# Performance work log

Measured on AMD Instinct MI355X. Metric: run time of the kernel, lower is better.

The kernel has to match this reference:

```python
import jax, jax.numpy as jnp
import numpy as np

NUM_LAYERS = 4
NUM_HEADS = 8
D_MODEL = 256
D_FF = 1024
UNC_THRESHOLD = 0.3
B, L = 2, 2048


def _layer_norm(x, g, b, eps=1e-5):
    m = jnp.mean(x, axis=-1, keepdims=True)
    v = jnp.mean((x - m) ** 2, axis=-1, keepdims=True)
    return (x - m) * jax.lax.rsqrt(v + eps) * g + b


def setup_inputs() -> dict:
    key = jax.random.key(0)
    ks = jax.random.split(key, 32)
    D, F, Ly = D_MODEL, D_FF, NUM_LAYERS
    w = lambda k, shape: jax.random.normal(k, shape, dtype=jnp.float32) * 0.02
    return {
        'x': jax.random.normal(ks[0], (B, L, D), dtype=jnp.float32),
        'Win': w(ks[1], (D, D)), 'bin_': jnp.zeros((D,), jnp.float32),
        'Wq': w(ks[2], (Ly, D, D)), 'bq': jnp.zeros((Ly, D), jnp.float32),
        'Wk': w(ks[3], (Ly, D, D)), 'bk': jnp.zeros((Ly, D), jnp.float32),
        'Wv': w(ks[4], (Ly, D, D)), 'bv': jnp.zeros((Ly, D), jnp.float32),
        'Wo': w(ks[5], (Ly, D, D)), 'bo': jnp.zeros((Ly, D), jnp.float32),
        'ev_scale': jnp.ones((Ly,), jnp.float32),
        'ev_bias': jnp.zeros((Ly,), jnp.float32),
        'W1': w(ks[6], (Ly, D, F)), 'b1': jnp.zeros((Ly, F), jnp.float32),
        'W2': w(ks[7], (Ly, F, D)), 'b2': jnp.zeros((Ly, D), jnp.float32),
        'n1g': jnp.ones((Ly, D), jnp.float32), 'n1b': jnp.zeros((Ly, D), jnp.float32),
        'n2g': jnp.ones((Ly, D), jnp.float32), 'n2b': jnp.zeros((Ly, D), jnp.float32),
        'fng': jnp.ones((D,), jnp.float32), 'fnb': jnp.zeros((D,), jnp.float32),
        'Wout': w(ks[8], (D, D)), 'bout': jnp.zeros((D,), jnp.float32),
    }


def _evidence_attention(x, Wq, bq, Wk, bk, Wv, bv, Wo, bo, scale, bias):
    b, l, d = x.shape
    hd = d // NUM_HEADS
    def heads(t):
        return t.reshape(b, l, NUM_HEADS, hd).transpose(0, 2, 1, 3)  # [B,H,L,hd]
    Q = heads(x @ Wq + bq)
    K = heads(x @ Wk + bk)
    V = heads(x @ Wv + bv)
    scores = jnp.einsum('bhqd,bhkd->bhqk', Q, K) / np.sqrt(hd).astype(np.float32)
    evidence = jnp.exp(scores) * scale + 1.0 + bias           # [B,H,L,L]
    denom = jnp.sum(evidence, axis=-1, keepdims=True)         # [B,H,L,1]
    uncertainty = (jnp.float32(l) / denom)[..., 0]            # [B,H,L]
    probs = evidence / denom
    attn = jnp.einsum('bhqk,bhkd->bhqd', probs, V)
    attn = attn.transpose(0, 2, 1, 3).reshape(b, l, d)
    return attn @ Wo + bo, uncertainty


def reference(x, Win, bin_, Wq, bq, Wk, bk, Wv, bv, Wo, bo, ev_scale, ev_bias,
              W1, b1, W2, b2, n1g, n1b, n2g, n2b, fng, fnb, Wout, bout):
    h = x @ Win + bin_
    total_unc = 0.0
    for i in range(NUM_LAYERS):
        attn_out, unc = _evidence_attention(
            _layer_norm(h, n1g[i], n1b[i]),
            Wq[i], bq[i], Wk[i], bk[i], Wv[i], bv[i], Wo[i], bo[i],
            ev_scale[i], ev_bias[i])
        h = h + attn_out
        ff = jax.nn.gelu(_layer_norm(h, n2g[i], n2b[i]) @ W1[i] + b1[i], approximate=False) @ W2[i] + b2[i]
        h = h + ff
        total_unc = total_unc + unc
    avg_unc = total_unc / NUM_LAYERS                          # [B,H,L]
    out = _layer_norm(h, fng, fnb) @ Wout + bout              # [B,L,D]
    should_abstain = avg_unc > UNC_THRESHOLD
    return out, avg_unc, should_abstain
```

## Files before the change

### kernel.cpp

```cpp
#include <hip/hip_runtime.h>
#include <hip/hip_bf16.h>
#include <math.h>

#define B_  2
#define L_  2048
#define D_  256
#define H_  8
#define HD_ 32
#define F_  1024
#define LY_ 4
#define M_  (B_*L_)

typedef __attribute__((ext_vector_type(8))) short bf16x8;
typedef __attribute__((ext_vector_type(4))) float f32x4;

static __device__ __forceinline__ short f2bf(float f) {
    return __builtin_bit_cast(short, __float2bfloat16(f));
}

static __device__ __forceinline__ void gload_lds16(const ushort* g, ushort* l) {
    __builtin_amdgcn_global_load_lds(
        (const __attribute__((address_space(1))) void*)g,
        (__attribute__((address_space(3))) void*)l, 16, 0, 0);
}

__global__ __launch_bounds__(256) void transpose_weights(
    const float* __restrict__ Win, const float* __restrict__ Wq,
    const float* __restrict__ Wk,  const float* __restrict__ Wv,
    const float* __restrict__ Wo,  const float* __restrict__ W1,
    const float* __restrict__ W2,  const float* __restrict__ Wout,
    ushort* __restrict__ T)
{
    const int bid = blockIdx.x;
    const float* src; ushort* dst; int K, N, tt;
    if (bid < 64)        { src = Win; dst = T; K = 256; N = 256; tt = bid; }
    else if (bid < 1088) {
        int i = bid - 64; int which = i >> 8; int l = (i >> 6) & 3; tt = i & 63;
        K = 256; N = 256;
        const float* s4[4] = {Wq, Wk, Wv, Wo};
        src = s4[which] + l * 65536;
        dst = T + 65536 * (1 + which * 4 + l);
    } else if (bid < 2112) {
        int i = bid - 1088; int l = i >> 8; tt = i & 255; K = 256; N = 1024;
        src = W1 + l * 262144; dst = T + 65536 * 17 + l * 262144;
    } else if (bid < 3136) {
        int i = bid - 2112; int l = i >> 8; tt = i & 255; K = 1024; N = 256;
        src = W2 + l * 262144; dst = T + 65536 * 17 + 1048576 + l * 262144;
    } else {
        src = Wout; dst = T + 65536 * 17 + 2097152; K = 256; N = 256; tt = bid - 3136;
    }
    const int ntn = N >> 5;
    const int tk = tt / ntn, tn = tt % ntn;
    __shared__ float ld[32][33];
    const int t = threadIdx.x;
    const int r = t >> 3, c4 = (t & 7) * 4;
    float4 v = *reinterpret_cast<const float4*>(&src[(size_t)(tk * 32 + r) * N + tn * 32 + c4]);
    ld[r][c4 + 0] = v.x; ld[r][c4 + 1] = v.y; ld[r][c4 + 2] = v.z; ld[r][c4 + 3] = v.w;
    __syncthreads();
    short4 o;
    o.x = f2bf(ld[c4 + 0][r]);
    o.y = f2bf(ld[c4 + 1][r]);
    o.z = f2bf(ld[c4 + 2][r]);
    o.w = f2bf(ld[c4 + 3][r]);
    *reinterpret_cast<short4*>(&dst[(size_t)(tn * 32 + r) * K + tk * 32 + c4]) = o;
}

__device__ __forceinline__ void gemm_core64(
    const ushort* __restrict__ A, const ushort* __restrict__ Wt, int K,
    int row0, int col0, ushort* sA, ushort* sW, f32x4 acc[2][2])
{
    const int tid  = threadIdx.x;
    const int lane = tid & 63;
    const int wid  = tid >> 6;
    const int wr = wid >> 1, wc = wid & 1;
    const int g = lane >> 4, nn = lane & 15;

    const int r0 = tid >> 3;
    const int sx = ((tid & 7) ^ (r0 & 7)) << 3;

    const ushort* Ap = &A[(size_t)(row0 + r0) * K + sx];
    const ushort* Wp = &Wt[(size_t)(col0 + r0) * K + sx];
    const size_t rstep = (size_t)32 * K;

    ushort* ldsA = sA + wid * 512;
    ushort* ldsW = sW + wid * 512;

    gload_lds16(Ap,         ldsA);
    gload_lds16(Ap + rstep, ldsA + 2048);
    gload_lds16(Wp,         ldsW);
    gload_lds16(Wp + rstep, ldsW + 2048);

    const int ra = (wr * 32 + nn) * 64, rb = ra + 16 * 64;
    const int rc = (wc * 32 + nn) * 64, rd = rc + 16 * 64;
    const int m7 = nn & 7;

    int cur = 0;
    __syncthreads();
    for (int k0 = 0; k0 < K; k0 += 64) {
        if (k0 + 64 < K) {
            ushort* lA = ldsA + (cur ^ 1) * 4096;
            ushort* lW = ldsW + (cur ^ 1) * 4096;
            gload_lds16(Ap + k0 + 64,         lA);
            gload_lds16(Ap + k0 + 64 + rstep, lA + 2048);
            gload_lds16(Wp + k0 + 64,         lW);
            gload_lds16(Wp + k0 + 64 + rstep, lW + 2048);
        }
        const ushort* a = sA + cur * 4096;
        const ushort* w = sW + cur * 4096;
#pragma unroll
        for (int sk = 0; sk < 2; ++sk) {
            const int sw = ((sk * 4 + g) ^ m7) << 3;
            bf16x8 a0 = *reinterpret_cast<const bf16x8*>(&a[ra + sw]);
            bf16x8 a1 = *reinterpret_cast<const bf16x8*>(&a[rb + sw]);
            bf16x8 w0 = *reinterpret_cast<const bf16x8*>(&w[rc + sw]);
            bf16x8 w1 = *reinterpret_cast<const bf16x8*>(&w[rd + sw]);
            acc[0][0] = __builtin_amdgcn_mfma_f32_16x16x32_bf16(a0, w0, acc[0][0], 0, 0, 0);
            acc[0][1] = __builtin_amdgcn_mfma_f32_16x16x32_bf16(a0, w1, acc[0][1], 0, 0, 0);
            acc[1][0] = __builtin_amdgcn_mfma_f32_16x16x32_bf16(a1, w0, acc[1][0], 0, 0, 0);
            acc[1][1] = __builtin_amdgcn_mfma_f32_16x16x32_bf16(a1, w1, acc[1][1], 0, 0, 0);
        }
        __syncthreads();
        cur ^= 1;
    }
}

__global__ __launch_bounds__(256) void gemm_first(
    const float* __restrict__ Hin, const ushort* __restrict__ Wt,
    const float* __restrict__ bias, float* __restrict__ Cout)
{
    __shared__ __align__(16) ushort sLN[64 * 264];
    __shared__ __align__(16) ushort sW[2 * 4096];
    const int row0 = blockIdx.y * 64, col0 = blockIdx.x * 64;
    const int tid  = threadIdx.x;
    const int lane = tid & 63;
    const int wid  = tid >> 6;
    const int wr = wid >> 1, wc = wid & 1;
    const int g = lane >> 4, nn = lane & 15;

    const int r0 = tid >> 3;
    const int sx = ((tid & 7) ^ (r0 & 7)) << 3;
    const ushort* Wp = &Wt[(size_t)(col0 + r0) * 256 + sx];
    ushort* ldsW = sW + wid * 512;
    gload_lds16(Wp,            ldsW);
    gload_lds16(Wp + 32 * 256, ldsW + 2048);

    const float4* hp = reinterpret_cast<const float4*>(Hin + (size_t)row0 * D_);
#pragma unroll
    for (int j = 0; j < 16; ++j) {
        const float4 v = hp[j * 256 + tid];
        short4 o = {f2bf(v.x), f2bf(v.y), f2bf(v.z), f2bf(v.w)};
        *reinterpret_cast<short4*>(&sLN[(j * 4 + wid) * 264 + lane * 4]) = o;
    }
    __syncthreads();

    const int ra = (wr * 32 + nn) * 264, rb = ra + 16 * 264;
    const int rc = (wc * 32 + nn) * 64,  rd = rc + 16 * 64;
    const int m7 = nn & 7;
    f32x4 acc[2][2] = {};

    int cur = 0;
#pragma unroll
    for (int k0 = 0; k0 < 256; k0 += 64) {
        if (k0 + 64 < 256) {
            ushort* lW = ldsW + (cur ^ 1) * 4096;
            gload_lds16(Wp + k0 + 64,            lW);
            gload_lds16(Wp + k0 + 64 + 32 * 256, lW + 2048);
        }
        const ushort* w = sW + cur * 4096;
#pragma unroll
        for (int sk = 0; sk < 2; ++sk) {
            const int ac = k0 + sk * 32 + g * 8;
            bf16x8 a0 = *reinterpret_cast<const bf16x8*>(&sLN[ra + ac]);
            bf16x8 a1 = *reinterpret_cast<const bf16x8*>(&sLN[rb + ac]);
            const int sw = ((sk * 4 + g) ^ m7) << 3;
            bf16x8 w0 = *reinterpret_cast<const bf16x8*>(&w[rc + sw]);
            bf16x8 w1 = *reinterpret_cast<const bf16x8*>(&w[rd + sw]);
            acc[0][0] = __builtin_amdgcn_mfma_f32_16x16x32_bf16(a0, w0, acc[0][0], 0, 0, 0);
            acc[0][1] = __builtin_amdgcn_mfma_f32_16x16x32_bf16(a0, w1, acc[0][1], 0, 0, 0);
            acc[1][0] = __builtin_amdgcn_mfma_f32_16x16x32_bf16(a1, w0, acc[1][0], 0, 0, 0);
            acc[1][1] = __builtin_amdgcn_mfma_f32_16x16x32_bf16(a1, w1, acc[1][1], 0, 0, 0);
        }
        __syncthreads();
        cur ^= 1;
    }

#pragma unroll
    for (int mi = 0; mi < 2; ++mi)
#pragma unroll
    for (int ni = 0; ni < 2; ++ni)
#pragma unroll
    for (int r = 0; r < 4; ++r) {
        const int m = row0 + wr * 32 + mi * 16 + g * 4 + r;
        const int c = col0 + wc * 32 + ni * 16 + nn;
        Cout[(size_t)m * D_ + c] = acc[mi][ni][r] + bias[c];
    }
}

__device__ __forceinline__ void gemm_core32(
    const ushort* __restrict__ A, const ushort* __restrict__ Wt, int K,
    int row0, int col0, ushort* sA, ushort* sW, f32x4 acc[2])
{
    const int tid  = threadIdx.x;
    const int lane = tid & 63;
    const int wid  = tid >> 6;
    const int wr = wid >> 1, wc = wid & 1;
    const int g = lane >> 4, nn = lane & 15;

    const int r0 = tid >> 3;
    const int sx = ((tid & 7) ^ (r0 & 7)) << 3;

    const ushort* Ap = &A[(size_t)(row0 + r0) * K + sx];
    const ushort* Wp = &Wt[(size_t)(col0 + r0) * K + sx];
    const size_t rstep = (size_t)32 * K;

    ushort* ldsA = sA + wid * 512;
    ushort* ldsW = sW + wid * 512;

    gload_lds16(Ap,         ldsA);
    gload_lds16(Wp,         ldsW);
    gload_lds16(Wp + rstep, ldsW + 2048);

    const int ra = (wr * 16 + nn) * 64;
    const int rc = (wc * 32 + nn) * 64, rd = rc + 16 * 64;
    const int m7 = nn & 7;

    int cur = 0;
    __syncthreads();
    for (int k0 = 0; k0 < K; k0 += 64) {
        if (k0 + 64 < K) {
            ushort* lA = ldsA + (cur ^ 1) * 2048;
            ushort* lW = ldsW + (cur ^ 1) * 4096;
            gload_lds16(Ap + k0 + 64,         lA);
            gload_lds16(Wp + k0 + 64,         lW);
            gload_lds16(Wp + k0 + 64 + rstep, lW + 2048);
        }
        const ushort* a = sA + cur * 2048;
        const ushort* w = sW + cur * 4096;
#pragma unroll
        for (int sk = 0; sk < 2; ++sk) {
            const int sw = ((sk * 4 + g) ^ m7) << 3;
            bf16x8 a0 = *reinterpret_cast<const bf16x8*>(&a[ra + sw]);
            bf16x8 w0 = *reinterpret_cast<const bf16x8*>(&w[rc + sw]);
            bf16x8 w1 = *reinterpret_cast<const bf16x8*>(&w[rd + sw]);
            acc[0] = __builtin_amdgcn_mfma_f32_16x16x32_bf16(a0, w0, acc[0], 0, 0, 0);
            acc[1] = __builtin_amdgcn_mfma_f32_16x16x32_bf16(a0, w1, acc[1], 0, 0, 0);
        }
        __syncthreads();
        cur ^= 1;
    }
}

__global__ __launch_bounds__(256) void gemm_res32(
    const ushort* __restrict__ A, const ushort* __restrict__ Wt,
    const float* __restrict__ bias, float* __restrict__ C, int K)
{
    __shared__ __align__(16) ushort sA[2 * 2048];
    __shared__ __align__(16) ushort sW[2 * 4096];
    const int row0 = blockIdx.y * 32, col0 = blockIdx.x * 64;
    f32x4 acc[2] = {};
    gemm_core32(A, Wt, K, row0, col0, sA, sW, acc);

    const int lane = threadIdx.x & 63;
    const int wid  = threadIdx.x >> 6;
    const int wr = wid >> 1, wc = wid & 1;
    const int g = lane >> 4, nn = lane & 15;
#pragma unroll
    for (int ni = 0; ni < 2; ++ni)
#pragma unroll
    for (int r = 0; r < 4; ++r) {
        const int m = row0 + wr * 16 + g * 4 + r;
        const int c = col0 + wc * 32 + ni * 16 + nn;
        C[(size_t)m * D_ + c] += acc[ni][r] + bias[c];
    }
}

__global__ __launch_bounds__(256) void gemm_out32(
    const ushort* __restrict__ A, const ushort* __restrict__ Wt,
    const float* __restrict__ bias, float* __restrict__ Cout)
{
    __shared__ __align__(16) ushort sA[2 * 2048];
    __shared__ __align__(16) ushort sW[2 * 4096];
    const int row0 = blockIdx.y * 32, col0 = blockIdx.x * 64;
    f32x4 acc[2] = {};
    gemm_core32(A, Wt, 256, row0, col0, sA, sW, acc);

    const int lane = threadIdx.x & 63;
    const int wid  = threadIdx.x >> 6;
    const int wr = wid >> 1, wc = wid & 1;
    const int g = lane >> 4, nn = lane & 15;
#pragma unroll
    for (int ni = 0; ni < 2; ++ni)
#pragma unroll
    for (int r = 0; r < 4; ++r) {
        const int m = row0 + wr * 16 + g * 4 + r;
        const int c = col0 + wc * 32 + ni * 16 + nn;
        Cout[(size_t)m * D_ + c] = acc[ni][r] + bias[c];
    }
}

template<int EPI, int OUTBF>
__global__ __launch_bounds__(256) void gemm_bf16(
    const ushort* __restrict__ A, const ushort* __restrict__ Wt,
    const float* __restrict__ bias, const float* __restrict__ res,
    void* __restrict__ Cout, int M, int N, int K)
{
    __shared__ __align__(16) ushort sA[2 * 4096];
    __shared__ __align__(16) ushort sW[2 * 4096];
    const int row0 = blockIdx.y * 64, col0 = blockIdx.x * 64;
    f32x4 acc[2][2] = {};
    gemm_core64(A, Wt, K, row0, col0, sA, sW, acc);

    const int lane = threadIdx.x & 63;
    const int wid  = threadIdx.x >> 6;
    const int wr = wid >> 1, wc = wid & 1;
    const int g = lane >> 4, nn = lane & 15;
#pragma unroll
    for (int mi = 0; mi < 2; ++mi)
#pragma unroll
    for (int ni = 0; ni < 2; ++ni)
#pragma unroll
    for (int r = 0; r < 4; ++r) {
        const int m = row0 + wr * 32 + mi * 16 + g * 4 + r;
        const int c = col0 + wc * 32 + ni * 16 + nn;
        float v = acc[mi][ni][r] + bias[c];
        if (EPI == 1) v = 0.5f * v * (1.0f + erff(v * 0.70710678118654752f));
        if (EPI == 2) v += res[(size_t)m * N + c];
        if (OUTBF) ((ushort*)Cout)[(size_t)m * N + c] = (ushort)f2bf(v);
        else       ((float*)Cout)[(size_t)m * N + c] = v;
    }
}

__global__ __launch_bounds__(256) void gemm_qkv(
    const ushort* __restrict__ A,
    const ushort* __restrict__ WqT, const ushort* __restrict__ WkT,
    const ushort* __restrict__ WvT,
    const float* __restrict__ bq, const float* __restrict__ bk,
    const float* __restrict__ bv,
    ushort* __restrict__ Qb, ushort* __restrict__ Kb, ushort* __restrict__ Vt)
{
    __shared__ __align__(16) ushort sA[2 * 4096];
    __shared__ __align__(16) ushort sW[2 * 4096];
    const int nb = blockIdx.x;
    const int wsel = nb >> 2;
    const int col0 = (nb & 3) * 64;
    const int row0 = blockIdx.y * 64;
    const ushort* Wt = (wsel == 0) ? WqT : (wsel == 1) ? WkT : WvT;
    const float* bias = (wsel == 0) ? bq : (wsel == 1) ? bk : bv;

    f32x4 acc[2][2] = {};
    gemm_core64(A, Wt, 256, row0, col0, sA, sW, acc);

    const int lane = threadIdx.x & 63;
    const int wid  = threadIdx.x >> 6;
    const int wr = wid >> 1, wc = wid & 1;
    const int g = lane >> 4, nn = lane & 15;
    ushort* QK = (wsel == 0) ? Qb : Kb;
#pragma unroll
    for (int mi = 0; mi < 2; ++mi)
#pragma unroll
    for (int ni = 0; ni < 2; ++ni)
#pragma unroll
    for (int r = 0; r < 4; ++r) {
        const int m = row0 + wr * 32 + mi * 16 + g * 4 + r;
        const int c = col0 + wc * 32 + ni * 16 + nn;
        const float v = acc[mi][ni][r] + bias[c];
        if (wsel < 2) {
            QK[(size_t)m * D_ + c] = (ushort)f2bf(v);
        } else {
            const int b = m >> 11, l = m & 2047;
            const int h = c >> 5,  d = c & 31;
            Vt[(size_t)((b * 8 + h) * 32 + d) * L_ + l] = (ushort)f2bf(v);
        }
    }
}

__global__ __launch_bounds__(256) void ln_kernel8(
    const float* __restrict__ x, const float* __restrict__ g,
    const float* __restrict__ b, ushort* __restrict__ y)
{
    const int tid  = threadIdx.x;
    const int row  = blockIdx.x * 8 + (tid >> 5);
    const int l    = tid & 31;
    const float* xp = x + (size_t)row * D_ + l * 8;

    float4 v0 = *reinterpret_cast<const float4*>(xp);
    float4 v1 = *reinterpret_cast<const float4*>(xp + 4);

    float s  = v0.x + v0.y + v0.z + v0.w + v1.x + v1.y + v1.z + v1.w;
    float s2 = v0.x*v0.x + v0.y*v0.y + v0.z*v0.z + v0.w*v0.w
             + v1.x*v1.x + v1.y*v1.y + v1.z*v1.z + v1.w*v1.w;
    s  += __shfl_xor(s, 1);  s  += __shfl_xor(s, 2);  s  += __shfl_xor(s, 4);
    s  += __shfl_xor(s, 8);  s  += __shfl_xor(s, 16);
    s2 += __shfl_xor(s2, 1); s2 += __shfl_xor(s2, 2); s2 += __shfl_xor(s2, 4);
    s2 += __shfl_xor(s2, 8); s2 += __shfl_xor(s2, 16);

    const float m   = s * (1.0f / D_);
    const float var = s2 * (1.0f / D_) - m * m;
    const float r   = rsqrtf(var + 1e-5f);

    const float4 g0 = reinterpret_cast<const float4*>(g)[l * 2];
    const float4 g1 = reinterpret_cast<const float4*>(g)[l * 2 + 1];
    const float4 b0 = reinterpret_cast<const float4*>(b)[l * 2];
    const float4 b1 = reinterpret_cast<const float4*>(b)[l * 2 + 1];

    short4 o0, o1;
    o0.x = f2bf((v0.x - m) * r * g0.x + b0.x);
    o0.y = f2bf((v0.y - m) * r * g0.y + b0.y);
    o0.z = f2bf((v0.z - m) * r * g0.z + b0.z);
    o0.w = f2bf((v0.w - m) * r * g0.w + b0.w);
    o1.x = f2bf((v1.x - m) * r * g1.x + b1.x);
    o1.y = f2bf((v1.y - m) * r * g1.y + b1.y);
    o1.z = f2bf((v1.z - m) * r * g1.z + b1.z);
    o1.w = f2bf((v1.w - m) * r * g1.w + b1.w);
    ushort* yp = y + (size_t)row * D_ + l * 8;
    *reinterpret_cast<short4*>(yp)     = o0;
    *reinterpret_cast<short4*>(yp + 4) = o1;
}

__global__ __launch_bounds__(256) void attn_mfma(
    const ushort* __restrict__ Qb, const ushort* __restrict__ Kb,
    const ushort* __restrict__ Vt, ushort* __restrict__ O,
    float* __restrict__ unc, const float* __restrict__ ev_scale,
    const float* __restrict__ ev_bias, int layer,
    float* __restrict__ out_unc, float* __restrict__ out_abst)
{
    const int bh = blockIdx.y;
    const int b  = bh >> 3;
    const int h  = bh & 7;
    const int tid  = threadIdx.x;
    const int wv   = tid >> 6;
    const int lane = tid & 63;
    const int g = lane >> 4;
    const int n = lane & 15;
    const int q  = blockIdx.x * 64 + wv * 16 + n;
    const float scale = ev_scale[layer];
    const float cb    = 1.0f + ev_bias[layer];
    const float isq   = 0.17677669529663687f;

    __shared__ __align__(16) ushort sK[2][64][40];
    __shared__ __align__(16) ushort sV[2][32][72];

    const size_t qk0 = (size_t)b * L_ * D_ + h * HD_;

    bf16x8 qf;
    {
        const bf16x8 qr = *reinterpret_cast<const bf16x8*>(&Qb[qk0 + (size_t)q * D_ + g * 8]);
#pragma unroll
        for (int j = 0; j < 8; ++j) {
            const float qv = __builtin_bit_cast(float, ((unsigned)(unsigned short)qr[j]) << 16);
            qf[j] = f2bf(qv * isq);
        }
    }
    bf16x8 ones;
#pragma unroll
    for (int j = 0; j < 8; ++j) ones[j] = (short)0x3F80;

    const int krow = tid >> 2, kch = (tid & 3) * 8;
    const int vrow = tid >> 3, vch = (tid & 7) * 8;
    const ushort* ksrc = Kb + qk0 + (size_t)krow * D_ + kch;
    const ushort* vsrc = Vt + (size_t)((b * 8 + h) * 32 + vrow) * L_ + vch;

    f32x4 acc0 = {0.f, 0.f, 0.f, 0.f};
    f32x4 acc1 = {0.f, 0.f, 0.f, 0.f};
    f32x4 accS = {0.f, 0.f, 0.f, 0.f};
    const f32x4 zero = {0.f, 0.f, 0.f, 0.f};

    bf16x8 kA = *reinterpret_cast<const bf16x8*>(ksrc);
    bf16x8 vA = *reinterpret_cast<const bf16x8*>(vsrc);
    bf16x8 kB = *reinterpret_cast<const bf16x8*>(ksrc + (size_t)64 * D_);
    bf16x8 vB = *reinterpret_cast<const bf16x8*>(vsrc + 64);

#define SYNC_BAR()                                                    \
    do {                                                              \
        asm volatile("s_waitcnt lgkmcnt(0)" ::: "memory");            \
        __builtin_amdgcn_s_barrier();                                 \
        asm volatile("" ::: "memory");                                \
    } while (0)

#define ATTN_TILE(BUF)                                                          \
    do {                                                                        \
        _Pragma("unroll")                                                       \
        for (int tt = 0; tt < 64; tt += 32) {                                   \
            bf16x8 kf0 = *reinterpret_cast<const bf16x8*>(&sK[BUF][tt + n][g * 8]);      \
            bf16x8 kf1 = *reinterpret_cast<const bf16x8*>(&sK[BUF][tt + 16 + n][g * 8]); \
            f32x4 s0 = __builtin_amdgcn_mfma_f32_16x16x32_bf16(kf0, qf, zero, 0, 0, 0);  \
            f32x4 s1 = __builtin_amdgcn_mfma_f32_16x16x32_bf16(kf1, qf, zero, 0, 0, 0);  \
            short4 va = *reinterpret_cast<const short4*>(&sV[BUF][n][tt + g * 4]);       \
            short4 vb = *reinterpret_cast<const short4*>(&sV[BUF][n][tt + 16 + g * 4]);  \
            short4 vc = *reinterpret_cast<const short4*>(&sV[BUF][n + 16][tt + g * 4]);  \
            short4 vd = *reinterpret_cast<const short4*>(&sV[BUF][n + 16][tt + 16 + g * 4]); \
            bf16x8 vf0 = {va.x, va.y, va.z, va.w, vb.x, vb.y, vb.z, vb.w};      \
            bf16x8 vf1 = {vc.x, vc.y, vc.z, vc.w, vd.x, vd.y, vd.z, vd.w};      \
            bf16x8 pa;                                                          \
            _Pragma("unroll")                                                   \
            for (int r = 0; r < 4; ++r) pa[r]     = f2bf(fmaf(__expf(s0[r]), scale, cb)); \
            _Pragma("unroll")                                                   \
            for (int r = 0; r < 4; ++r) pa[r + 4] = f2bf(fmaf(__expf(s1[r]), scale, cb)); \
            acc0 = __builtin_amdgcn_mfma_f32_16x16x32_bf16(vf0, pa, acc0, 0, 0, 0); \
            acc1 = __builtin_amdgcn_mfma_f32_16x16x32_bf16(vf1, pa, acc1, 0, 0, 0); \
            accS = __builtin_amdgcn_mfma_f32_16x16x32_bf16(ones, pa, accS, 0, 0, 0); \
        }                                                                       \
    } while (0)

    for (int t = 0; t < L_; t += 128) {
        *reinterpret_cast<bf16x8*>(&sK[0][krow][kch]) = kA;
        *reinterpret_cast<bf16x8*>(&sV[0][vrow][vch]) = vA;
        if (t + 128 < L_) {
            kA = *reinterpret_cast<const bf16x8*>(ksrc + (size_t)(t + 128) * D_);
            vA = *reinterpret_cast<const bf16x8*>(vsrc + (t + 128));
        }
        SYNC_BAR();
        ATTN_TILE(0);

        *reinterpret_cast<bf16x8*>(&sK[1][krow][kch]) = kB;
        *reinterpret_cast<bf16x8*>(&sV[1][vrow][vch]) = vB;
        if (t + 192 < L_) {
            kB = *reinterpret_cast<const bf16x8*>(ksrc + (size_t)(t + 192) * D_);
            vB = *reinterpret_cast<const bf16x8*>(vsrc + (t + 192));
        }
        SYNC_BAR();
        ATTN_TILE(1);
    }
#undef ATTN_TILE
#undef SYNC_BAR

    const float inv = 1.0f / accS[0];

    ushort* op = &O[qk0 + (size_t)q * D_ + g * 4];
    short4 o0 = {f2bf(acc0[0] * inv), f2bf(acc0[1] * inv), f2bf(acc0[2] * inv), f2bf(acc0[3] * inv)};
    short4 o1 = {f2bf(acc1[0] * inv), f2bf(acc1[1] * inv), f2bf(acc1[2] * inv), f2bf(acc1[3] * inv)};
    *reinterpret_cast<short4*>(op)      = o0;
    *reinterpret_cast<short4*>(op + 16) = o1;

    if (g == 0) {
        const float u = (float)L_ * inv;
        const int uidx = bh * L_ + q;
        if (layer == 0) {
            unc[uidx] = u;
        } else if (layer < LY_ - 1) {
            unc[uidx] += u;
        } else {
            const float avg = (unc[uidx] + u) * 0.25f;
            out_unc[uidx]  = avg;
            out_abst[uidx] = (avg > 0.3f) ? 1.0f : 0.0f;
        }
    }
}

extern "C" void kernel_launch(void* const* d_in, const int* in_sizes, int n_in,
                              void* d_out, int out_size, void* d_ws, size_t ws_size,
                              hipStream_t stream)
{
    const float* x    = (const float*)d_in[0];
    const float* Win  = (const float*)d_in[1];
    const float* bin_ = (const float*)d_in[2];
    const float* Wq   = (const float*)d_in[3];
    const float* bq   = (const float*)d_in[4];
    const float* Wk   = (const float*)d_in[5];
    const float* bk   = (const float*)d_in[6];
    const float* Wv   = (const float*)d_in[7];
    const float* bv   = (const float*)d_in[8];
    const float* Wo   = (const float*)d_in[9];
    const float* bo   = (const float*)d_in[10];
    const float* evs  = (const float*)d_in[11];
    const float* evb  = (const float*)d_in[12];
    const float* W1   = (const float*)d_in[13];
    const float* b1   = (const float*)d_in[14];
    const float* W2   = (const float*)d_in[15];
    const float* b2   = (const float*)d_in[16];
    const float* n1g  = (const float*)d_in[17];
    const float* n1b  = (const float*)d_in[18];
    const float* n2g  = (const float*)d_in[19];
    const float* n2b  = (const float*)d_in[20];
    const float* fng  = (const float*)d_in[21];
    const float* fnb  = (const float*)d_in[22];
    const float* Wout = (const float*)d_in[23];
    const float* bout = (const float*)d_in[24];

    char* ws = (char*)d_ws;
    float*  h    = (float*) (ws);
    ushort* tmpb = (ushort*)(ws + (4  << 20));
    ushort* Qb   = (ushort*)(ws + (6  << 20));
    ushort* Kb   = (ushort*)(ws + (8  << 20));
    ushort* Vt   = (ushort*)(ws + (10 << 20));
    ushort* Ob   = (ushort*)(ws + (12 << 20));
    ushort* ffb  = (ushort*)(ws + (6  << 20));
    float*  unc  = (float*) (ws + (14 << 20));
    ushort* T    = (ushort*)(ws + (15 << 20));

    ushort* winT  = T;
    ushort* woutT = T + 65536 * 17 + 2097152;

    float* out_main = (float*)d_out;
    float* out_unc  = out_main + M_ * D_;
    float* out_abst = out_unc + B_ * H_ * L_;

    const dim3 blk(256);
    const dim3 g64(4, 64);
    const dim3 g32(4, 128);
    const dim3 g1024(16, 64);
    const dim3 gqkv(12, 64);
    const dim3 gattn(L_ / 64, B_ * H_);
    const dim3 gln(M_ / 8);

    transpose_weights<<<3200, blk, 0, stream>>>(Win, Wq, Wk, Wv, Wo, W1, W2, Wout, T);
    gemm_first<<<g64, blk, 0, stream>>>(x, winT, bin_, h);

    for (int i = 0; i < LY_; ++i) {
        ushort* wqT = T + 65536 * (1 + i);
        ushort* wkT = T + 65536 * (5 + i);
        ushort* wvT = T + 65536 * (9 + i);
        ushort* woT = T + 65536 * (13 + i);
        ushort* w1T = T + 65536 * 17 + i * 262144;
        ushort* w2T = T + 65536 * 17 + 1048576 + i * 262144;

        ln_kernel8<<<gln, blk, 0, stream>>>(h, n1g + i * D_, n1b + i * D_, tmpb);
        gemm_qkv<<<gqkv, blk, 0, stream>>>(tmpb, wqT, wkT, wvT,
                                           bq + i * D_, bk + i * D_, bv + i * D_,
                                           Qb, Kb, Vt);
        attn_mfma<<<gattn, blk, 0, stream>>>(Qb, Kb, Vt, Ob, unc, evs, evb, i,
                                             out_unc, out_abst);
        gemm_res32<<<g32, blk, 0, stream>>>(Ob, woT, bo + i * D_, h, 256);
        ln_kernel8<<<gln, blk, 0, stream>>>(h, n2g + i * D_, n2b + i * D_, tmpb);
        gemm_bf16<1, 1><<<g1024, blk, 0, stream>>>(tmpb, w1T, b1 + i * F_, nullptr, ffb, M_, F_, D_);
        gemm_res32<<<g32, blk, 0, stream>>>(ffb, w2T, b2 + i * D_, h, 1024);
    }

    ln_kernel8<<<gln, blk, 0, stream>>>(h, fng, fnb, tmpb);
    gemm_out32<<<g32, blk, 0, stream>>>(tmpb, woutT, bout, out_main);
}
```

Before: 284.6 us.

## Triple-buffer GEMM K-loop with vmcnt waits and single barrier; use exp2 in attention

Every GEMM core moves from double-buffered LDS with two __syncthreads per step to a three-stage ring. Loads run two stages ahead, guarded by explicit s_waitcnt vmcnt counts and one barrier per iteration, and K becomes a template parameter so the loop trip count is known at compile time. The attention kernel folds log2(e) into the query scale and uses exp2f in place of __expf. This is meant to hide global-to-LDS latency and cut barrier stalls, at the cost of more LDS per block (possible occupancy loss) and reliance on hand-counted vmcnt values being correct.

```diff
diff --git a/kernel.cpp b/kernel.cpp
--- a/kernel.cpp
+++ b/kernel.cpp
@@ -22,6 +22,17 @@
     __builtin_amdgcn_global_load_lds(
         (const __attribute__((address_space(1))) void*)g,
         (__attribute__((address_space(3))) void*)l, 16, 0, 0);
+}
+
+template<int N> static __device__ __forceinline__ void s_wait_vm() {
+    if constexpr (N == 0) asm volatile("s_waitcnt vmcnt(0) lgkmcnt(0)" ::: "memory");
+    if constexpr (N == 2) asm volatile("s_waitcnt vmcnt(2) lgkmcnt(0)" ::: "memory");
+    if constexpr (N == 3) asm volatile("s_waitcnt vmcnt(3) lgkmcnt(0)" ::: "memory");
+    if constexpr (N == 4) asm volatile("s_waitcnt vmcnt(4) lgkmcnt(0)" ::: "memory");
+}
+static __device__ __forceinline__ void bar3() {
+    __builtin_amdgcn_s_barrier();
+    __builtin_amdgcn_sched_barrier(0);
 }
 
 __global__ __launch_bounds__(256) void transpose_weights(
@@ -65,10 +76,12 @@
     *reinterpret_cast<short4*>(&dst[(size_t)(tn * 32 + r) * K + tk * 32 + c4]) = o;
 }
 
-__device__ __forceinline__ void gemm_core64(
-    const ushort* __restrict__ A, const ushort* __restrict__ Wt, int K,
+template<int K>
+__device__ __forceinline__ void gemm_core64t(
+    const ushort* __restrict__ A, const ushort* __restrict__ Wt,
     int row0, int col0, ushort* sA, ushort* sW, f32x4 acc[2][2])
 {
+    constexpr int NK = K / 64;
     const int tid  = threadIdx.x;
     const int lane = tid & 63;
     const int wid  = tid >> 6;
@@ -85,28 +98,32 @@
     ushort* ldsA = sA + wid * 512;
     ushort* ldsW = sW + wid * 512;
 
-    gload_lds16(Ap,         ldsA);
-    gload_lds16(Ap + rstep, ldsA + 2048);
-    gload_lds16(Wp,         ldsW);
-    gload_lds16(Wp + rstep, ldsW + 2048);
+    auto stage = [&](int s, int b) {
+        ushort* lA = ldsA + b * 4096;
+        ushort* lW = ldsW + b * 4096;
+        gload_lds16(Ap + s * 64,         lA);
+        gload_lds16(Ap + s * 64 + rstep, lA + 2048);
+        gload_lds16(Wp + s * 64,         lW);
+        gload_lds16(Wp + s * 64 + rstep, lW + 2048);
+    };
+    stage(0, 0);
+    if (NK > 1) stage(1, 1);
 
     const int ra = (wr * 32 + nn) * 64, rb = ra + 16 * 64;
     const int rc = (wc * 32 + nn) * 64, rd = rc + 16 * 64;
     const int m7 = nn & 7;
 
-    int cur = 0;
-    __syncthreads();
-    for (int k0 = 0; k0 < K; k0 += 64) {
-        if (k0 + 64 < K) {
-            ushort* lA = ldsA + (cur ^ 1) * 4096;
-            ushort* lW = ldsW + (cur ^ 1) * 4096;
-            gload_lds16(Ap + k0 + 64,         lA);
-            gload_lds16(Ap + k0 + 64 + rstep, lA + 2048);
-            gload_lds16(Wp + k0 + 64,         lW);
-            gload_lds16(Wp + k0 + 64 + rstep, lW + 2048);
-        }
-        const ushort* a = sA + cur * 4096;
-        const ushort* w = sW + cur * 4096;
+    int bC = 0, bI = 2;
+    for (int k = 0; k < NK; ++k) {
+        if (k + 1 < NK) s_wait_vm<4>();
+        else            s_wait_vm<0>();
+        bar3();
+        if (k + 2 < NK) {
+            stage(k + 2, bI);
+            bI = (bI == 2) ? 0 : bI + 1;
+        }
+        const ushort* a = sA + bC * 4096;
+        const ushort* w = sW + bC * 4096;
 #pragma unroll
         for (int sk = 0; sk < 2; ++sk) {
             const int sw = ((sk * 4 + g) ^ m7) << 3;
@@ -119,8 +136,7 @@
             acc[1][0] = __builtin_amdgcn_mfma_f32_16x16x32_bf16(a1, w0, acc[1][0], 0, 0, 0);
             acc[1][1] = __builtin_amdgcn_mfma_f32_16x16x32_bf16(a1, w1, acc[1][1], 0, 0, 0);
         }
-        __syncthreads();
-        cur ^= 1;
+        bC = (bC == 2) ? 0 : bC + 1;
     }
 }
 
@@ -129,7 +145,7 @@
     const float* __restrict__ bias, float* __restrict__ Cout)
 {
     __shared__ __align__(16) ushort sLN[64 * 264];
-    __shared__ __align__(16) ushort sW[2 * 4096];
+    __shared__ __align__(16) ushort sW[3 * 4096];
     const int row0 = blockIdx.y * 64, col0 = blockIdx.x * 64;
     const int tid  = threadIdx.x;
     const int lane = tid & 63;
@@ -141,8 +157,14 @@
     const int sx = ((tid & 7) ^ (r0 & 7)) << 3;
     const ushort* Wp = &Wt[(size_t)(col0 + r0) * 256 + sx];
     ushort* ldsW = sW + wid * 512;
-    gload_lds16(Wp,            ldsW);
-    gload_lds16(Wp + 32 * 256, ldsW + 2048);
+
+    auto stageW = [&](int s, int b) {
+        ushort* lW = ldsW + b * 4096;
+        gload_lds16(Wp + s * 64,            lW);
+        gload_lds16(Wp + s * 64 + 32 * 256, lW + 2048);
+    };
+    stageW(0, 0);
+    stageW(1, 1);
 
     const float4* hp = reinterpret_cast<const float4*>(Hin + (size_t)row0 * D_);
 #pragma unroll
@@ -151,25 +173,25 @@
         short4 o = {f2bf(v.x), f2bf(v.y), f2bf(v.z), f2bf(v.w)};
         *reinterpret_cast<short4*>(&sLN[(j * 4 + wid) * 264 + lane * 4]) = o;
     }
-    __syncthreads();
 
     const int ra = (wr * 32 + nn) * 264, rb = ra + 16 * 264;
     const int rc = (wc * 32 + nn) * 64,  rd = rc + 16 * 64;
     const int m7 = nn & 7;
     f32x4 acc[2][2] = {};
 
-    int cur = 0;
-#pragma unroll
-    for (int k0 = 0; k0 < 256; k0 += 64) {
-        if (k0 + 64 < 256) {
-            ushort* lW = ldsW + (cur ^ 1) * 4096;
-            gload_lds16(Wp + k0 + 64,            lW);
-            gload_lds16(Wp + k0 + 64 + 32 * 256, lW + 2048);
-        }
-        const ushort* w = sW + cur * 4096;
+    int bC = 0, bI = 2;
+    for (int k = 0; k < 4; ++k) {
+        if (k + 1 < 4) s_wait_vm<2>();
+        else           s_wait_vm<0>();
+        bar3();
+        if (k + 2 < 4) {
+            stageW(k + 2, bI);
+            bI = (bI == 2) ? 0 : bI + 1;
+        }
+        const ushort* w = sW + bC * 4096;
 #pragma unroll
         for (int sk = 0; sk < 2; ++sk) {
-            const int ac = k0 + sk * 32 + g * 8;
+            const int ac = k * 64 + sk * 32 + g * 8;
             bf16x8 a0 = *reinterpret_cast<const bf16x8*>(&sLN[ra + ac]);
             bf16x8 a1 = *reinterpret_cast<const bf16x8*>(&sLN[rb + ac]);
             const int sw = ((sk * 4 + g) ^ m7) << 3;
@@ -180,8 +202,7 @@
             acc[1][0] = __builtin_amdgcn_mfma_f32_16x16x32_bf16(a1, w0, acc[1][0], 0, 0, 0);
             acc[1][1] = __builtin_amdgcn_mfma_f32_16x16x32_bf16(a1, w1, acc[1][1], 0, 0, 0);
         }
-        __syncthreads();
-        cur ^= 1;
+        bC = (bC == 2) ? 0 : bC + 1;
     }
 
 #pragma unroll
@@ -196,10 +217,12 @@
     }
 }
 
-__device__ __forceinline__ void gemm_core32(
-    const ushort* __restrict__ A, const ushort* __restrict__ Wt, int K,
+template<int K>
+__device__ __forceinline__ void gemm_core32t(
+    const ushort* __restrict__ A, const ushort* __restrict__ Wt,
     int row0, int col0, ushort* sA, ushort* sW, f32x4 acc[2])
 {
+    constexpr int NK = K / 64;
     const int tid  = threadIdx.x;
     const int lane = tid & 63;
     const int wid  = tid >> 6;
@@ -216,26 +239,29 @@
     ushort* ldsA = sA + wid * 512;
     ushort* ldsW = sW + wid * 512;
 
-    gload_lds16(Ap,         ldsA);
-    gload_lds16(Wp,         ldsW);
-    gload_lds16(Wp + rstep, ldsW + 2048);
+    auto stage = [&](int s, int b) {
+        gload_lds16(Ap + s * 64,         ldsA + b * 2048);
+        gload_lds16(Wp + s * 64,         ldsW + b * 4096);
+        gload_lds16(Wp + s * 64 + rstep, ldsW + b * 4096 + 2048);
+    };
+    stage(0, 0);
+    if (NK > 1) stage(1, 1);
 
     const int ra = (wr * 16 + nn) * 64;
     const int rc = (wc * 32 + nn) * 64, rd = rc + 16 * 64;
     const int m7 = nn & 7;
 
-    int cur = 0;
-    __syncthreads();
-    for (int k0 = 0; k0 < K; k0 += 64) {
-        if (k0 + 64 < K) {
-            ushort* lA = ldsA + (cur ^ 1) * 2048;
-            ushort* lW = ldsW + (cur ^ 1) * 4096;
-            gload_lds16(Ap + k0 + 64,         lA);
-            gload_lds16(Wp + k0 + 64,         lW);
-            gload_lds16(Wp + k0 + 64 + rstep, lW + 2048);
-        }
-        const ushort* a = sA + cur * 2048;
-        const ushort* w = sW + cur * 4096;
+    int bC = 0, bI = 2;
+    for (int k = 0; k < NK; ++k) {
+        if (k + 1 < NK) s_wait_vm<3>();
+        else            s_wait_vm<0>();
+        bar3();
+        if (k + 2 < NK) {
+            stage(k + 2, bI);
+            bI = (bI == 2) ? 0 : bI + 1;
+        }
+        const ushort* a = sA + bC * 2048;
+        const ushort* w = sW + bC * 4096;
 #pragma unroll
         for (int sk = 0; sk < 2; ++sk) {
             const int sw = ((sk * 4 + g) ^ m7) << 3;
@@ -245,20 +271,20 @@
             acc[0] = __builtin_amdgcn_mfma_f32_16x16x32_bf16(a0, w0, acc[0], 0, 0, 0);
             acc[1] = __builtin_amdgcn_mfma_f32_16x16x32_bf16(a0, w1, acc[1], 0, 0, 0);
         }
-        __syncthreads();
-        cur ^= 1;
-    }
-}
-
+        bC = (bC == 2) ? 0 : bC + 1;
+    }
+}
+
+template<int K>
 __global__ __launch_bounds__(256) void gemm_res32(
     const ushort* __restrict__ A, const ushort* __restrict__ Wt,
-    const float* __restrict__ bias, float* __restrict__ C, int K)
-{
-    __shared__ __align__(16) ushort sA[2 * 2048];
-    __shared__ __align__(16) ushort sW[2 * 4096];
+    const float* __restrict__ bias, float* __restrict__ C)
+{
+    __shared__ __align__(16) ushort sA[3 * 2048];
+    __shared__ __align__(16) ushort sW[3 * 4096];
     const int row0 = blockIdx.y * 32, col0 = blockIdx.x * 64;
     f32x4 acc[2] = {};
-    gemm_core32(A, Wt, K, row0, col0, sA, sW, acc);
+    gemm_core32t<K>(A, Wt, row0, col0, sA, sW, acc);
 
     const int lane = threadIdx.x & 63;
     const int wid  = threadIdx.x >> 6;
@@ -278,11 +304,11 @@
     const ushort* __restrict__ A, const ushort* __restrict__ Wt,
     const float* __restrict__ bias, float* __restrict__ Cout)
 {
-    __shared__ __align__(16) ushort sA[2 * 2048];
-    __shared__ __align__(16) ushort sW[2 * 4096];
+    __shared__ __align__(16) ushort sA[3 * 2048];
+    __shared__ __align__(16) ushort sW[3 * 4096];
     const int row0 = blockIdx.y * 32, col0 = blockIdx.x * 64;
     f32x4 acc[2] = {};
-    gemm_core32(A, Wt, 256, row0, col0, sA, sW, acc);
+    gemm_core32t<256>(A, Wt, row0, col0, sA, sW, acc);
 
     const int lane = threadIdx.x & 63;
     const int wid  = threadIdx.x >> 6;
@@ -302,13 +328,13 @@
 __global__ __launch_bounds__(256) void gemm_bf16(
     const ushort* __restrict__ A, const ushort* __restrict__ Wt,
     const float* __restrict__ bias, const float* __restrict__ res,
-    void* __restrict__ Cout, int M, int N, int K)
-{
-    __shared__ __align__(16) ushort sA[2 * 4096];
-    __shared__ __align__(16) ushort sW[2 * 4096];
+    void* __restrict__ Cout, int M, int N)
+{
+    __shared__ __align__(16) ushort sA[3 * 4096];
+    __shared__ __align__(16) ushort sW[3 * 4096];
     const int row0 = blockIdx.y * 64, col0 = blockIdx.x * 64;
     f32x4 acc[2][2] = {};
-    gemm_core64(A, Wt, K, row0, col0, sA, sW, acc);
+    gemm_core64t<256>(A, Wt, row0, col0, sA, sW, acc);
 
     const int lane = threadIdx.x & 63;
     const int wid  = threadIdx.x >> 6;
@@ -338,8 +364,8 @@
     const float* __restrict__ bv,
     ushort* __restrict__ Qb, ushort* __restrict__ Kb, ushort* __restrict__ Vt)
 {
-    __shared__ __align__(16) ushort sA[2 * 4096];
-    __shared__ __align__(16) ushort sW[2 * 4096];
+    __shared__ __align__(16) ushort sA[3 * 4096];
+    __shared__ __align__(16) ushort sW[3 * 4096];
     const int nb = blockIdx.x;
     const int wsel = nb >> 2;
     const int col0 = (nb & 3) * 64;
@@ -348,7 +374,7 @@
     const float* bias = (wsel == 0) ? bq : (wsel == 1) ? bk : bv;
 
     f32x4 acc[2][2] = {};
-    gemm_core64(A, Wt, 256, row0, col0, sA, sW, acc);
+    gemm_core64t<256>(A, Wt, row0, col0, sA, sW, acc);
 
     const int lane = threadIdx.x & 63;
     const int wid  = threadIdx.x >> 6;
@@ -435,7 +461,7 @@
     const int q  = blockIdx.x * 64 + wv * 16 + n;
     const float scale = ev_scale[layer];
     const float cb    = 1.0f + ev_bias[layer];
-    const float isq   = 0.17677669529663687f;
+    const float isql  = 0.17677669529663687f * 1.4426950408889634f;
 
     __shared__ __align__(16) ushort sK[2][64][40];
     __shared__ __align__(16) ushort sV[2][32][72];
@@ -448,7 +474,7 @@
 #pragma unroll
         for (int j = 0; j < 8; ++j) {
             const float qv = __builtin_bit_cast(float, ((unsigned)(unsigned short)qr[j]) << 16);
-            qf[j] = f2bf(qv * isq);
+            qf[j] = f2bf(qv * isql);
         }
     }
     bf16x8 ones;
@@ -493,9 +519,9 @@
             bf16x8 vf1 = {vc.x, vc.y, vc.z, vc.w, vd.x, vd.y, vd.z, vd.w};      \
             bf16x8 pa;                                                          \
             _Pragma("unroll")                                                   \
-            for (int r = 0; r < 4; ++r) pa[r]     = f2bf(fmaf(__expf(s0[r]), scale, cb)); \
+            for (int r = 0; r < 4; ++r) pa[r]     = f2bf(fmaf(exp2f(s0[r]), scale, cb)); \
             _Pragma("unroll")                                                   \
-            for (int r = 0; r < 4; ++r) pa[r + 4] = f2bf(fmaf(__expf(s1[r]), scale, cb)); \
+            for (int r = 0; r < 4; ++r) pa[r + 4] = f2bf(fmaf(exp2f(s1[r]), scale, cb)); \
             acc0 = __builtin_amdgcn_mfma_f32_16x16x32_bf16(vf0, pa, acc0, 0, 0, 0); \
             acc1 = __builtin_amdgcn_mfma_f32_16x16x32_bf16(vf1, pa, acc1, 0, 0, 0); \
             accS = __builtin_amdgcn_mfma_f32_16x16x32_bf16(ones, pa, accS, 0, 0, 0); \
@@ -620,10 +646,10 @@
                                            Qb, Kb, Vt);
         attn_mfma<<<gattn, blk, 0, stream>>>(Qb, Kb, Vt, Ob, unc, evs, evb, i,
                                              out_unc, out_abst);
-        gemm_res32<<<g32, blk, 0, stream>>>(Ob, woT, bo + i * D_, h, 256);
+        gemm_res32<256><<<g32, blk, 0, stream>>>(Ob, woT, bo + i * D_, h);
         ln_kernel8<<<gln, blk, 0, stream>>>(h, n2g + i * D_, n2b + i * D_, tmpb);
-        gemm_bf16<1, 1><<<g1024, blk, 0, stream>>>(tmpb, w1T, b1 + i * F_, nullptr, ffb, M_, F_, D_);
-        gemm_res32<<<g32, blk, 0, stream>>>(ffb, w2T, b2 + i * D_, h, 1024);
+        gemm_bf16<1, 1><<<g1024, blk, 0, stream>>>(tmpb, w1T, b1 + i * F_, nullptr, ffb, M_, F_);
+        gemm_res32<1024><<<g32, blk, 0, stream>>>(ffb, w2T, b2 + i * D_, h);
     }
 
     ln_kernel8<<<gln, blk, 0, stream>>>(h, fng, fnb, tmpb);
```

New measurement: 300.1 us. 5.4% more time.
